# Performance work log

Measured on AMD Instinct MI355X. Metric: run time of the kernel, lower is better.

## Reference

```python
import jax, jax.numpy as jnp
import numpy as np

N_HEAD = 12

def setup_inputs() -> dict:
    key = jax.random.key(0)
    ks = jax.random.split(key, 5)
    B, T, C = 2, 2048, 768
    s = 1.0 / np.sqrt(C)
    return {
        "x": jax.random.normal(ks[0], (B, T, C), dtype=jnp.float32),
        "W_qkv": jax.random.normal(ks[1], (C, 3 * C), dtype=jnp.float32) * s,
        "b_qkv": jnp.zeros((3 * C,), dtype=jnp.float32),
        "W_proj": jax.random.normal(ks[2], (C, C), dtype=jnp.float32) * s,
        "b_proj": jnp.zeros((C,), dtype=jnp.float32),
    }

def reference(x, W_qkv, b_qkv, W_proj, b_proj):
    B, T, C = x.shape
    H = N_HEAD
    D = C // H
    qkv = x @ W_qkv + b_qkv                      # [B,T,3C]
    qkv = qkv.reshape(B, T, 3, H, D)
    q = jnp.transpose(qkv[:, :, 0], (0, 2, 1, 3))  # [B,H,T,D]
    k = jnp.transpose(qkv[:, :, 1], (0, 2, 1, 3))
    v = jnp.transpose(qkv[:, :, 2], (0, 2, 1, 3))
    scale = 1.0 / np.sqrt(D).astype(np.float32)
    att = jnp.einsum('bhqd,bhkd->bhqk', q, k) * scale  # [B,H,T,T]
    causal = jnp.tril(jnp.ones((T, T), dtype=bool))
    att = jnp.where(causal, att, -jnp.inf)
    att = jax.nn.softmax(att, axis=-1)
    out = jnp.einsum('bhqk,bhkd->bhqd', att, v)   # [B,H,T,D]
    out = jnp.transpose(out, (0, 2, 1, 3)).reshape(B, T, C)
    return out @ W_proj + b_proj
```

## Files before the change

kernel.cpp:

```cpp
#include <hip/hip_runtime.h>
#include <stdint.h>

typedef short short8 __attribute__((ext_vector_type(8)));
typedef short short4v __attribute__((ext_vector_type(4)));
typedef float f32x4 __attribute__((ext_vector_type(4)));
typedef unsigned int u32x2 __attribute__((ext_vector_type(2)));
typedef unsigned int u32x4 __attribute__((ext_vector_type(4)));
typedef unsigned short u16;
typedef unsigned int u32;

#define T_ 2048
#define QK_SCALE 0.180336878f

__device__ inline u16 f2bf(float f) {
  unsigned u = __builtin_bit_cast(unsigned, f);
  u += 0x7fffu + ((u >> 16) & 1u);
  return (u16)(u >> 16);
}

__device__ inline u32 cvt_pk_bf16(float lo, float hi) {
  u32 r;
  asm("v_cvt_pk_bf16_f32 %0, %1, %2" : "=v"(r) : "v"(lo), "v"(hi));
  return r;
}

__device__ inline f32x4 mfma_bf16(short8 a, short8 b, f32x4 c) {
  return __builtin_amdgcn_mfma_f32_16x16x32_bf16(a, b, c, 0, 0, 0);
}

__device__ inline void gload16(const u16* g, u16* l) {
  __builtin_amdgcn_global_load_lds(
      (const __attribute__((address_space(1))) void*)g,
      (__attribute__((address_space(3))) void*)l, 16, 0, 0);
}


__device__ inline void tile_transpose(const float* __restrict__ W, u16* __restrict__ Wt,
                                      int R, int Ccols, int c0, int r0, int t,
                                      float (*tile)[33]) {
  int tr = t >> 3, tc = (t & 7) * 4;
  float4 v = *(const float4*)&W[(size_t)(r0 + tr) * Ccols + c0 + tc];
  tile[tr][tc + 0] = v.x; tile[tr][tc + 1] = v.y;
  tile[tr][tc + 2] = v.z; tile[tr][tc + 3] = v.w;
  __syncthreads();
  short4v o;
#pragma unroll
  for (int i = 0; i < 4; ++i) o[i] = (short)f2bf(tile[tc + i][tr]);
  *(short4v*)&Wt[(size_t)(c0 + tr) * R + r0 + tc] = o;
}

__global__ __launch_bounds__(256) void prep_kernel(const float* __restrict__ x,
                                                   const float* __restrict__ Wqkv,
                                                   const float* __restrict__ Wproj,
                                                   u16* __restrict__ xb,
                                                   u16* __restrict__ wqkvT,
                                                   u16* __restrict__ wprojT) {
  __shared__ float tile[32][33];
  int bid = blockIdx.x, t = threadIdx.x;
  if (bid < 3072) {
    int i = (bid * 256 + t) * 4;
    float4 v = *(const float4*)&x[i];
    short4v o;
    o[0] = (short)f2bf(v.x); o[1] = (short)f2bf(v.y);
    o[2] = (short)f2bf(v.z); o[3] = (short)f2bf(v.w);
    *(short4v*)&xb[i] = o;
  } else if (bid < 3072 + 1728) {
    int t2 = bid - 3072;
    tile_transpose(Wqkv, wqkvT, 768, 2304, (t2 % 72) * 32, (t2 / 72) * 32, t, tile);
  } else {
    int t3 = bid - 4800;
    tile_transpose(Wproj, wprojT, 768, 768, (t3 % 24) * 32, (t3 / 24) * 32, t, tile);
  }
}


template <int MODE, int MTILE>
__global__ __launch_bounds__(256) void gemm_kernel(const u16* __restrict__ A,
                                                   const u16* __restrict__ Bt,
                                                   const float* __restrict__ bias,
                                                   u16* __restrict__ qb,
                                                   u16* __restrict__ kb,
                                                   u16* __restrict__ vpb,
                                                   float* __restrict__ out) {
  constexpr int MF = MTILE / 32;
  __shared__ u16 S[MTILE * 64 + 8192];
  u16* As = S;
  u16* Bs = S + MTILE * 64;
  int tid = threadIdx.x, w = tid >> 6, l = tid & 63, lg = l >> 4, lr = l & 15;
  int nwg = gridDim.x * gridDim.y;
  int hw = blockIdx.y * gridDim.x + blockIdx.x;
  int logical = (hw & 7) * (nwg >> 3) + (hw >> 3);
  int n0 = (logical % gridDim.x) * 128, m0 = (logical / gridDim.x) * MTILE;
  int wm = (w >> 1) * (MTILE / 2), wn = (w & 1) * 64;
  f32x4 acc[MF][4] = {};
  int rsub = l >> 3;
  int sc = ((l & 7) ^ rsub) * 8;
  for (int kt = 0; kt < 12; ++kt) {
    int k0 = kt * 64;
    __syncthreads();
#pragma unroll
    for (int j = 0; j < MF; ++j) {
      int row = w * (MTILE / 4) + j * 8 + rsub;
      gload16(&A[(size_t)(m0 + row) * 768 + k0 + sc], &As[(w * MF + j) * 512]);
    }
#pragma unroll
    for (int j = 0; j < 4; ++j) {
      int row = w * 32 + j * 8 + rsub;
      gload16(&Bt[(size_t)(n0 + row) * 768 + k0 + sc], &Bs[(w * 4 + j) * 512]);
    }
    __syncthreads();
    short8 a[MF][2], b[4][2];
#pragma unroll
    for (int h = 0; h < 2; ++h) {
#pragma unroll
      for (int mf = 0; mf < MF; ++mf) {
        int cw = ((h * 4 + lg) ^ (lr & 7)) * 8;
        a[mf][h] = *(const short8*)&As[(wm + mf * 16 + lr) * 64 + cw];
      }
#pragma unroll
      for (int nf = 0; nf < 4; ++nf) {
        int cw = ((h * 4 + lg) ^ (lr & 7)) * 8;
        b[nf][h] = *(const short8*)&Bs[(wn + nf * 16 + lr) * 64 + cw];
      }
    }
#pragma unroll
    for (int h = 0; h < 2; ++h)
#pragma unroll
      for (int mf = 0; mf < MF; ++mf)
#pragma unroll
        for (int nf = 0; nf < 4; ++nf)
          acc[mf][nf] = mfma_bf16(a[mf][h], b[nf][h], acc[mf][nf]);
  }

  if constexpr (MODE == 0) {
    int sec = (n0 >= 1536) ? 2 : (n0 >= 768 ? 1 : 0);
    int ncol0 = n0 - sec * 768;
    if (sec < 2) {
#pragma unroll
      for (int nf = 0; nf < 4; ++nf) {
        int nn = wn + nf * 16 + lr;
        float bv = bias[n0 + nn];
        int c = ncol0 + nn;
        int hh = c >> 6, d = c & 63;
#pragma unroll
        for (int mf = 0; mf < MF; ++mf)
#pragma unroll
          for (int rr = 0; rr < 4; ++rr) {
            int m = m0 + wm + mf * 16 + 4 * lg + rr;
            int bb = m >> 11, tt = m & 2047;
            int bh = bb * 12 + hh;
            float v = acc[mf][nf][rr] + bv;
            if (sec == 0) qb[((size_t)bh * T_ + tt) * 64 + d] = f2bf(v * QK_SCALE);
            else          kb[((size_t)bh * T_ + tt) * 64 + d] = f2bf(v);
          }
      }
    } else {
      __syncthreads();
#pragma unroll
      for (int nf = 0; nf < 4; ++nf) {
        int row = wn + nf * 16 + lr;
        float bv = bias[n0 + row];
        int swz = (row & 7) << 3;
#pragma unroll
        for (int mf = 0; mf < MF; ++mf) {
          int pcol0 = wm + (mf >> 1) * 32 + 8 * lg + 4 * (mf & 1);
          u32x2 pk;
          pk[0] = cvt_pk_bf16(acc[mf][nf][0] + bv, acc[mf][nf][1] + bv);
          pk[1] = cvt_pk_bf16(acc[mf][nf][2] + bv, acc[mf][nf][3] + bv);
          *(u32x2*)&S[row * MTILE + (pcol0 ^ swz)] = pk;
        }
      }
      __syncthreads();
      constexpr int CPT = MTILE / 2;
      int rowo = tid >> 1, half = tid & 1;
      int c = ncol0 + rowo;
      int d = c & 63, hh = c >> 6;
      int bh = (m0 >> 11) * 12 + hh;
      u16* dst = vpb + ((size_t)bh * 64 + d) * T_ + (m0 & 2047) + half * CPT;
      int swzo = (rowo & 7) << 3;
#pragma unroll
      for (int i = 0; i < CPT / 8; ++i) {
        int col = half * CPT + i * 8;
        uint4 v = *(const uint4*)&S[rowo * MTILE + (col ^ swzo)];
        *(uint4*)&dst[i * 8] = v;
      }
    }
  } else {
#pragma unroll
    for (int nf = 0; nf < 4; ++nf) {
      int n = n0 + wn + nf * 16 + lr;
      float bv = bias[n];
#pragma unroll
      for (int mf = 0; mf < MF; ++mf)
#pragma unroll
        for (int rr = 0; rr < 4; ++rr) {
          int m = m0 + wm + mf * 16 + 4 * lg + rr;
          out[(size_t)m * 768 + n] = acc[mf][nf][rr] + bv;
        }
    }
  }
}


__global__ __launch_bounds__(256) void attn_kernel(const u16* __restrict__ Q,
                                                   const u16* __restrict__ K,
                                                   const u16* __restrict__ Vp,
                                                   u16* __restrict__ O) {
  __shared__ u16 sh[16384];
  int tid = threadIdx.x;
  int w = tid >> 6, l = tid & 63, lg = l >> 4, lr = l & 15;
  int idx = blockIdx.x;
  int head = idx % 24;
  int qblk = 31 - idx / 24;
  int b = head / 12, h = head % 12;
  int q0 = qblk * 64;
  int q0w = q0 + w * 16;
  const u16* Qb = Q + (size_t)head * T_ * 64;
  const u16* Kb = K + (size_t)head * T_ * 64;
  const u16* Vb = Vp + (size_t)head * 64 * T_;

  short8 qf0 = *(const short8*)&Qb[(size_t)(q0w + lr) * 64 + 8 * lg];
  short8 qf1 = *(const short8*)&Qb[(size_t)(q0w + lr) * 64 + 32 + 8 * lg];

  f32x4 ao[4] = {};
  float lrow = 0.f;
  int rsub = l >> 3;
  int scs = ((l & 7) ^ rsub) * 8;
  const int nt = qblk + 1;

#pragma unroll
  for (int j = 0; j < 2; ++j) {
    int ci = w * 2 + j;
    int row = ci * 8 + rsub;
    gload16(&Kb[(size_t)row * 64 + scs], &sh[ci * 512]);
    gload16(&Vb[(size_t)row * T_ + scs], &sh[8192 + ci * 512]);
  }
  __syncthreads();

  for (int t = 0; t < nt; ++t) {
    int cur = t & 1;
    int k0 = t * 64;
    if (t + 1 < nt) {
      int k1 = k0 + 64;
#pragma unroll
      for (int j = 0; j < 2; ++j) {
        int ci = w * 2 + j;
        int row = ci * 8 + rsub;
        gload16(&Kb[(size_t)(k1 + row) * 64 + scs], &sh[(cur ^ 1) * 4096 + ci * 512]);
        gload16(&Vb[(size_t)row * T_ + k1 + scs], &sh[8192 + (cur ^ 1) * 4096 + ci * 512]);
      }
    }
    if (k0 <= q0w + 15) {
      const u16* ks = sh + cur * 4096;
      const u16* vs = sh + 8192 + cur * 4096;
      short8 ka0[4], ka1[4], va0[4], va1[4];
#pragma unroll
      for (int kg = 0; kg < 4; ++kg) {
        ka0[kg] = *(const short8*)&ks[(kg * 16 + lr) * 64 + ((lg ^ (lr & 7)) * 8)];
        ka1[kg] = *(const short8*)&ks[(kg * 16 + lr) * 64 + (((4 + lg) ^ (lr & 7)) * 8)];
      }
#pragma unroll
      for (int dt = 0; dt < 4; ++dt) {
        va0[dt] = *(const short8*)&vs[(dt * 16 + lr) * 64 + ((lg ^ (lr & 7)) * 8)];
        va1[dt] = *(const short8*)&vs[(dt * 16 + lr) * 64 + (((4 + lg) ^ (lr & 7)) * 8)];
      }
      f32x4 sm[4];
      __builtin_amdgcn_s_setprio(1);
#pragma unroll
      for (int kg = 0; kg < 4; ++kg) {
        f32x4 z = {};
        z = mfma_bf16(ka0[kg], qf0, z);
        z = mfma_bf16(ka1[kg], qf1, z);
        sm[kg] = z;
      }
      __builtin_amdgcn_s_setprio(0);
      float sv[16];
      float ps = 0.f;
      if (t == nt - 1) {
        int qa = q0w + lr;
#pragma unroll
        for (int kg = 0; kg < 4; ++kg)
#pragma unroll
          for (int rr = 0; rr < 4; ++rr) {
            int key = k0 + kg * 16 + 4 * lg + rr;
            float x = (key <= qa) ? sm[kg][rr] : -1e30f;
            float p = __builtin_amdgcn_exp2f(x);
            sv[kg * 4 + rr] = p;
            ps += p;
          }
      } else {
#pragma unroll
        for (int kg = 0; kg < 4; ++kg)
#pragma unroll
          for (int rr = 0; rr < 4; ++rr) {
            float p = __builtin_amdgcn_exp2f(sm[kg][rr]);
            sv[kg * 4 + rr] = p;
            ps += p;
          }
      }
      lrow += ps;
      short8 pb[2];
#pragma unroll
      for (int c2 = 0; c2 < 2; ++c2) {
        u32x4 uu;
        uu[0] = cvt_pk_bf16(sv[c2 * 8 + 0], sv[c2 * 8 + 1]);
        uu[1] = cvt_pk_bf16(sv[c2 * 8 + 2], sv[c2 * 8 + 3]);
        uu[2] = cvt_pk_bf16(sv[c2 * 8 + 4], sv[c2 * 8 + 5]);
        uu[3] = cvt_pk_bf16(sv[c2 * 8 + 6], sv[c2 * 8 + 7]);
        pb[c2] = __builtin_bit_cast(short8, uu);
      }
      __builtin_amdgcn_s_setprio(1);
#pragma unroll
      for (int dt = 0; dt < 4; ++dt) {
        ao[dt] = mfma_bf16(va0[dt], pb[0], ao[dt]);
        ao[dt] = mfma_bf16(va1[dt], pb[1], ao[dt]);
      }
      __builtin_amdgcn_s_setprio(0);
    }
    __syncthreads();
  }

  lrow += __shfl_xor(lrow, 16);
  lrow += __shfl_xor(lrow, 32);
  u16* ow = sh + w * 1152;
  float inv = 1.0f / lrow;
#pragma unroll
  for (int dt = 0; dt < 4; ++dt) {
    u32x2 pk;
    pk[0] = cvt_pk_bf16(ao[dt][0] * inv, ao[dt][1] * inv);
    pk[1] = cvt_pk_bf16(ao[dt][2] * inv, ao[dt][3] * inv);
    *(u32x2*)&ow[lr * 72 + dt * 16 + 4 * lg] = pk;
  }
  __syncthreads();
  int r = l >> 2, hc = l & 3;
  const u16* srow = sh + w * 1152 + r * 72 + hc * 16;
  u16* dst = O + ((size_t)(b * T_ + q0w + r)) * 768 + h * 64 + hc * 16;
  *(uint4*)&dst[0] = *(const uint4*)&srow[0];
  *(uint4*)&dst[8] = *(const uint4*)&srow[8];
}


extern "C" void kernel_launch(void* const* d_in, const int* in_sizes, int n_in,
                              void* d_out, int out_size, void* d_ws, size_t ws_size,
                              hipStream_t stream) {
  const float* x     = (const float*)d_in[0];
  const float* Wqkv  = (const float*)d_in[1];
  const float* bqkv  = (const float*)d_in[2];
  const float* Wproj = (const float*)d_in[3];
  const float* bproj = (const float*)d_in[4];
  float* out = (float*)d_out;
  char* ws = (char*)d_ws;
  u16* xb     = (u16*)(ws);
  u16* wqkvT  = (u16*)(ws + 6291456);
  u16* wprojT = (u16*)(ws + 9830400);
  u16* qb     = (u16*)(ws + 11010048);
  u16* kb     = (u16*)(ws + 17301504);
  u16* vpb    = (u16*)(ws + 23592960);
  u16* ob     = (u16*)(ws + 29884416);

  prep_kernel<<<5376, 256, 0, stream>>>(x, Wqkv, Wproj, xb, wqkvT, wprojT);
  gemm_kernel<0, 64><<<dim3(18, 64), 256, 0, stream>>>(xb, wqkvT, bqkv, qb, kb, vpb, nullptr);
  attn_kernel<<<768, 256, 0, stream>>>(qb, kb, vpb, ob);
  gemm_kernel<1, 64><<<dim3(6, 64), 256, 0, stream>>>(ob, wprojT, bproj, nullptr, nullptr, nullptr, out);
}
```

Measured before the change: 78.45 us.

## Split attention key tiles across wave pairs with LDS reduction

The attention block grows from 4 to 8 waves. Each pair of waves shares a 16-row query slice and splits every 64-key tile into two 32-key halves, with partial outputs and row sums combined through shared memory at the end. This doubles the parallelism per block and halves each wave's serial MFMA and exp chain, and each wave now issues one K/V tile load instead of two. In exchange it adds an LDS reduction, larger blocks that may lower occupancy, and a softmax without a running max that still relies on bounded scores.

```diff
diff --git a/kernel.cpp b/kernel.cpp
--- a/kernel.cpp
+++ b/kernel.cpp
@@ -202,19 +202,20 @@
 }
 
 
-__global__ __launch_bounds__(256) void attn_kernel(const u16* __restrict__ Q,
+__global__ __launch_bounds__(512) void attn_kernel(const u16* __restrict__ Q,
                                                    const u16* __restrict__ K,
                                                    const u16* __restrict__ Vp,
                                                    u16* __restrict__ O) {
   __shared__ u16 sh[16384];
   int tid = threadIdx.x;
   int w = tid >> 6, l = tid & 63, lg = l >> 4, lr = l & 15;
+  int i = w >> 1, j = w & 1;
   int idx = blockIdx.x;
   int head = idx % 24;
   int qblk = 31 - idx / 24;
   int b = head / 12, h = head % 12;
   int q0 = qblk * 64;
-  int q0w = q0 + w * 16;
+  int q0w = q0 + i * 16;
   const u16* Qb = Q + (size_t)head * T_ * 64;
   const u16* Kb = K + (size_t)head * T_ * 64;
   const u16* Vb = Vp + (size_t)head * 64 * T_;
@@ -228,12 +229,10 @@
   int scs = ((l & 7) ^ rsub) * 8;
   const int nt = qblk + 1;
 
-#pragma unroll
-  for (int j = 0; j < 2; ++j) {
-    int ci = w * 2 + j;
-    int row = ci * 8 + rsub;
-    gload16(&Kb[(size_t)row * 64 + scs], &sh[ci * 512]);
-    gload16(&Vb[(size_t)row * T_ + scs], &sh[8192 + ci * 512]);
+  {
+    int row = w * 8 + rsub;
+    gload16(&Kb[(size_t)row * 64 + scs], &sh[w * 512]);
+    gload16(&Vb[(size_t)row * T_ + scs], &sh[8192 + w * 512]);
   }
   __syncthreads();
 
@@ -242,79 +241,69 @@
     int k0 = t * 64;
     if (t + 1 < nt) {
       int k1 = k0 + 64;
-#pragma unroll
-      for (int j = 0; j < 2; ++j) {
-        int ci = w * 2 + j;
-        int row = ci * 8 + rsub;
-        gload16(&Kb[(size_t)(k1 + row) * 64 + scs], &sh[(cur ^ 1) * 4096 + ci * 512]);
-        gload16(&Vb[(size_t)row * T_ + k1 + scs], &sh[8192 + (cur ^ 1) * 4096 + ci * 512]);
-      }
-    }
-    if (k0 <= q0w + 15) {
+      int row = w * 8 + rsub;
+      gload16(&Kb[(size_t)(k1 + row) * 64 + scs], &sh[(cur ^ 1) * 4096 + w * 512]);
+      gload16(&Vb[(size_t)row * T_ + k1 + scs], &sh[8192 + (cur ^ 1) * 4096 + w * 512]);
+    }
+    if (k0 + 32 * j <= q0w + 15) {
       const u16* ks = sh + cur * 4096;
       const u16* vs = sh + 8192 + cur * 4096;
-      short8 ka0[4], ka1[4], va0[4], va1[4];
-#pragma unroll
-      for (int kg = 0; kg < 4; ++kg) {
-        ka0[kg] = *(const short8*)&ks[(kg * 16 + lr) * 64 + ((lg ^ (lr & 7)) * 8)];
-        ka1[kg] = *(const short8*)&ks[(kg * 16 + lr) * 64 + (((4 + lg) ^ (lr & 7)) * 8)];
-      }
-#pragma unroll
-      for (int dt = 0; dt < 4; ++dt) {
-        va0[dt] = *(const short8*)&vs[(dt * 16 + lr) * 64 + ((lg ^ (lr & 7)) * 8)];
-        va1[dt] = *(const short8*)&vs[(dt * 16 + lr) * 64 + (((4 + lg) ^ (lr & 7)) * 8)];
-      }
-      f32x4 sm[4];
+      short8 ka0[2], ka1[2], va[4];
+#pragma unroll
+      for (int g = 0; g < 2; ++g) {
+        int kg = 2 * j + g;
+        ka0[g] = *(const short8*)&ks[(kg * 16 + lr) * 64 + ((lg ^ (lr & 7)) * 8)];
+        ka1[g] = *(const short8*)&ks[(kg * 16 + lr) * 64 + (((4 + lg) ^ (lr & 7)) * 8)];
+      }
+#pragma unroll
+      for (int dt = 0; dt < 4; ++dt)
+        va[dt] = *(const short8*)&vs[(dt * 16 + lr) * 64 + (((4 * j + lg) ^ (lr & 7)) * 8)];
+      f32x4 sm[2];
       __builtin_amdgcn_s_setprio(1);
 #pragma unroll
-      for (int kg = 0; kg < 4; ++kg) {
+      for (int g = 0; g < 2; ++g) {
         f32x4 z = {};
-        z = mfma_bf16(ka0[kg], qf0, z);
-        z = mfma_bf16(ka1[kg], qf1, z);
-        sm[kg] = z;
+        z = mfma_bf16(ka0[g], qf0, z);
+        z = mfma_bf16(ka1[g], qf1, z);
+        sm[g] = z;
       }
       __builtin_amdgcn_s_setprio(0);
-      float sv[16];
+      float sv[8];
       float ps = 0.f;
-      if (t == nt - 1) {
+      bool needmask = (t == nt - 1) && (32 * j + 31 > 16 * i);
+      if (needmask) {
         int qa = q0w + lr;
 #pragma unroll
-        for (int kg = 0; kg < 4; ++kg)
+        for (int g = 0; g < 2; ++g)
 #pragma unroll
           for (int rr = 0; rr < 4; ++rr) {
-            int key = k0 + kg * 16 + 4 * lg + rr;
-            float x = (key <= qa) ? sm[kg][rr] : -1e30f;
+            int key = k0 + (2 * j + g) * 16 + 4 * lg + rr;
+            float x = (key <= qa) ? sm[g][rr] : -1e30f;
             float p = __builtin_amdgcn_exp2f(x);
-            sv[kg * 4 + rr] = p;
+            sv[g * 4 + rr] = p;
             ps += p;
           }
       } else {
 #pragma unroll
-        for (int kg = 0; kg < 4; ++kg)
+        for (int g = 0; g < 2; ++g)
 #pragma unroll
           for (int rr = 0; rr < 4; ++rr) {
-            float p = __builtin_amdgcn_exp2f(sm[kg][rr]);
-            sv[kg * 4 + rr] = p;
+            float p = __builtin_amdgcn_exp2f(sm[g][rr]);
+            sv[g * 4 + rr] = p;
             ps += p;
           }
       }
       lrow += ps;
-      short8 pb[2];
-#pragma unroll
-      for (int c2 = 0; c2 < 2; ++c2) {
-        u32x4 uu;
-        uu[0] = cvt_pk_bf16(sv[c2 * 8 + 0], sv[c2 * 8 + 1]);
-        uu[1] = cvt_pk_bf16(sv[c2 * 8 + 2], sv[c2 * 8 + 3]);
-        uu[2] = cvt_pk_bf16(sv[c2 * 8 + 4], sv[c2 * 8 + 5]);
-        uu[3] = cvt_pk_bf16(sv[c2 * 8 + 6], sv[c2 * 8 + 7]);
-        pb[c2] = __builtin_bit_cast(short8, uu);
-      }
+      u32x4 uu;
+      uu[0] = cvt_pk_bf16(sv[0], sv[1]);
+      uu[1] = cvt_pk_bf16(sv[2], sv[3]);
+      uu[2] = cvt_pk_bf16(sv[4], sv[5]);
+      uu[3] = cvt_pk_bf16(sv[6], sv[7]);
+      short8 pb = __builtin_bit_cast(short8, uu);
       __builtin_amdgcn_s_setprio(1);
 #pragma unroll
-      for (int dt = 0; dt < 4; ++dt) {
-        ao[dt] = mfma_bf16(va0[dt], pb[0], ao[dt]);
-        ao[dt] = mfma_bf16(va1[dt], pb[1], ao[dt]);
-      }
+      for (int dt = 0; dt < 4; ++dt)
+        ao[dt] = mfma_bf16(va[dt], pb, ao[dt]);
       __builtin_amdgcn_s_setprio(0);
     }
     __syncthreads();
@@ -322,21 +311,37 @@
 
   lrow += __shfl_xor(lrow, 16);
   lrow += __shfl_xor(lrow, 32);
-  u16* ow = sh + w * 1152;
-  float inv = 1.0f / lrow;
-#pragma unroll
-  for (int dt = 0; dt < 4; ++dt) {
-    u32x2 pk;
-    pk[0] = cvt_pk_bf16(ao[dt][0] * inv, ao[dt][1] * inv);
-    pk[1] = cvt_pk_bf16(ao[dt][2] * inv, ao[dt][3] * inv);
-    *(u32x2*)&ow[lr * 72 + dt * 16 + 4 * lg] = pk;
+
+  float* aoL = (float*)sh;
+  float* lrL = (float*)(sh + 8192);
+  if (j == 1) {
+#pragma unroll
+    for (int dt = 0; dt < 4; ++dt)
+      *(f32x4*)&aoL[(i * 64 + l) * 16 + dt * 4] = ao[dt];
+    lrL[i * 64 + l] = lrow;
   }
   __syncthreads();
-  int r = l >> 2, hc = l & 3;
-  const u16* srow = sh + w * 1152 + r * 72 + hc * 16;
-  u16* dst = O + ((size_t)(b * T_ + q0w + r)) * 768 + h * 64 + hc * 16;
-  *(uint4*)&dst[0] = *(const uint4*)&srow[0];
-  *(uint4*)&dst[8] = *(const uint4*)&srow[8];
+  if (j == 0) {
+#pragma unroll
+    for (int dt = 0; dt < 4; ++dt)
+      ao[dt] += *(const f32x4*)&aoL[(i * 64 + l) * 16 + dt * 4];
+    lrow += lrL[i * 64 + l];
+    u16* ow = sh + 9216 + i * 1152;
+    float inv = 1.0f / lrow;
+#pragma unroll
+    for (int dt = 0; dt < 4; ++dt) {
+      u32x2 pk;
+      pk[0] = cvt_pk_bf16(ao[dt][0] * inv, ao[dt][1] * inv);
+      pk[1] = cvt_pk_bf16(ao[dt][2] * inv, ao[dt][3] * inv);
+      *(u32x2*)&ow[lr * 72 + dt * 16 + 4 * lg] = pk;
+    }
+    asm volatile("s_waitcnt lgkmcnt(0)" ::: "memory");
+    int r = l >> 2, hc = l & 3;
+    const u16* srow = sh + 9216 + i * 1152 + r * 72 + hc * 16;
+    u16* dst = O + ((size_t)(b * T_ + q0w + r)) * 768 + h * 64 + hc * 16;
+    *(uint4*)&dst[0] = *(const uint4*)&srow[0];
+    *(uint4*)&dst[8] = *(const uint4*)&srow[8];
+  }
 }
 
 
@@ -360,6 +365,6 @@
 
   prep_kernel<<<5376, 256, 0, stream>>>(x, Wqkv, Wproj, xb, wqkvT, wprojT);
   gemm_kernel<0, 64><<<dim3(18, 64), 256, 0, stream>>>(xb, wqkvT, bqkv, qb, kb, vpb, nullptr);
-  attn_kernel<<<768, 256, 0, stream>>>(qb, kb, vpb, ob);
+  attn_kernel<<<768, 512, 0, stream>>>(qb, kb, vpb, ob);
   gemm_kernel<1, 64><<<dim3(6, 64), 256, 0, stream>>>(ob, wprojT, bproj, nullptr, nullptr, nullptr, out);
 }
```

After: 77.15 us. No clear change (-1.7%).
